# Optimization experiments

Hardware: AMD Instinct MI355X
Metric: run time of the kernel (lower is better)

## Reference

```python
import jax, jax.numpy as jnp
import numpy as np

# Binary (sign) weight linear: y = x @ sign(W)^T + b

def _binarize(w):
    # sign with sign(0) mapped to +1, as in typical BinaryLinear impls
    return jnp.where(w >= 0, 1.0, -1.0).astype(w.dtype)

def setup_inputs() -> dict:
    key = jax.random.key(0)
    ks = jax.random.split(key, 7)
    B = 65536
    x = jax.random.normal(ks[0], (B, 28, 28), dtype=jnp.float32)
    W1 = jax.random.normal(ks[1], (1000, 784), dtype=jnp.float32) * 0.05
    b1 = jax.random.normal(ks[2], (1000,), dtype=jnp.float32) * 0.01
    W2 = jax.random.normal(ks[3], (500, 1000), dtype=jnp.float32) * 0.05
    b2 = jax.random.normal(ks[4], (500,), dtype=jnp.float32) * 0.01
    W3 = jax.random.normal(ks[5], (10, 500), dtype=jnp.float32) * 0.05
    b3 = jax.random.normal(ks[6], (10,), dtype=jnp.float32) * 0.01
    return {"x": x, "W1": W1, "b1": b1, "W2": W2, "b2": b2, "W3": W3, "b3": b3}

def reference(x, W1, b1, W2, b2, W3, b3):
    h = x.reshape(x.shape[0], -1)                      # [B, 784]
    h = jnp.maximum(h @ _binarize(W1).T + b1, 0.0)     # [B, 1000]
    h = jnp.maximum(h @ _binarize(W2).T + b2, 0.0)     # [B, 500]
    return h @ _binarize(W3).T + b3                    # [B, 10]
```

## Files before the change

### kernel.cpp

```cpp
#include <hip/hip_runtime.h>
#include <stdint.h>


typedef __attribute__((ext_vector_type(8))) short bf16x8;
typedef __attribute__((ext_vector_type(4))) float f32x4;

typedef const __attribute__((address_space(1))) unsigned int* as1_u32p;
typedef __attribute__((address_space(3))) unsigned int* as3_u32p;

__device__ __forceinline__ void glds16(const void* g, void* l) {
  __builtin_amdgcn_global_load_lds((as1_u32p)g, (as3_u32p)l, 16, 0, 0);
}

__device__ __forceinline__ unsigned short f2bf(float f) {
  union { float f; unsigned u; } c;
  c.f = f;
  unsigned u = c.u;
  u += 0x7FFFu + ((u >> 16) & 1u);
  return (unsigned short)(u >> 16);
}

__device__ __forceinline__ void binarize_one(const float* __restrict__ src,
                                             int Ns, int Ks, short* __restrict__ dst,
                                             int Kp, int idx, int total) {
  if (idx >= total) return;
  int n = idx / Kp;
  int k = idx - n * Kp;
  short v = 0;
  if (n < Ns && k < Ks)
    v = (src[n * Ks + k] >= 0.0f) ? (short)0x3F80 : (short)0xBF80;
  dst[idx] = v;
}

__global__ void prep_kernel(const float* __restrict__ X, short* __restrict__ Xp,
                            const float* __restrict__ W1, short* __restrict__ W1b,
                            const float* __restrict__ W2, short* __restrict__ W2b,
                            const float* __restrict__ W3, short* __restrict__ W3b) {
  constexpr int C0 = 26624;
  constexpr int C1 = C0 + 3328;
  constexpr int C2 = C1 + 2048;
  const int bid = blockIdx.x;
  if (bid < C0) {
    const int g = bid * 256 + threadIdx.x;
    const int row = g / 104;
    const int c = (g - row * 104) * 8;
    short tmp[8];
    if (c < 784) {
      const float* s = X + (size_t)row * 784 + c;
      float4 f0 = *(const float4*)s;
      float4 f1 = *(const float4*)(s + 4);
      tmp[0] = (short)f2bf(f0.x); tmp[1] = (short)f2bf(f0.y);
      tmp[2] = (short)f2bf(f0.z); tmp[3] = (short)f2bf(f0.w);
      tmp[4] = (short)f2bf(f1.x); tmp[5] = (short)f2bf(f1.y);
      tmp[6] = (short)f2bf(f1.z); tmp[7] = (short)f2bf(f1.w);
    } else {
#pragma unroll
      for (int i = 0; i < 8; ++i) tmp[i] = 0;
    }
    *(bf16x8*)(Xp + (size_t)row * 832 + c) = *(bf16x8*)(tmp);
  } else if (bid < C1) {
    binarize_one(W1, 1000, 784, W1b, 832, (bid - C0) * 256 + threadIdx.x, 1024 * 832);
  } else if (bid < C2) {
    binarize_one(W2, 500, 1000, W2b, 1024, (bid - C1) * 256 + threadIdx.x, 512 * 1024);
  } else {
    binarize_one(W3, 10, 500, W3b, 512, (bid - C2) * 256 + threadIdx.x, 16 * 512);
  }
}

template <int KP, int NKT, int NP, int NR, int NT>
__global__ __launch_bounds__(512, 4)
void gemm128x256(const short* __restrict__ A, const short* __restrict__ Wb,
                 const float* __restrict__ bias, short* __restrict__ Hout) {
  __shared__ short Abuf[3][128 * 32];
  __shared__ short Bbuf[3][256 * 32];

  constexpr int NWG8 = (512 * NT) >> 3;
  const int d = blockIdx.x;
  const int lid = (d & 7) * NWG8 + (d >> 3);
  const int mi = lid / NT;
  const int ni = lid - mi * NT;
  const int m0 = mi << 7;
  const int n0 = ni << 8;
  const int start = (ni * NKT) / NT;

  const int tid = threadIdx.x;
  const int lane = tid & 63;
  const int w = tid >> 6;
  const int wm = w >> 2;
  const int wn = w & 3;
  const int l15 = lane & 15;
  const int quad = lane >> 4;

  const int srow = tid >> 2;
  const int sslot = tid & 3;
  const int gcol = ((sslot ^ ((srow >> 1) & 3)) << 3);
  const short* ag = A + (size_t)(m0 + srow) * KP + gcol;
  const short* bg = Wb + (size_t)(n0 + srow) * KP + gcol;
  const int ldsw = w << 9;

  auto stageA = [&](int pb, int kit) {
    glds16(ag + kit * 32, &Abuf[pb][ldsw]);
  };
  auto stageB = [&](int pb, int kit) {
    const short* s = bg + kit * 32;
    glds16(s, &Bbuf[pb][ldsw]);
    glds16(s + (size_t)128 * KP, &Bbuf[pb][ldsw + 4096]);
  };

  const int sl = (quad ^ ((l15 >> 1) & 3)) << 3;
  const int abase = ((wm << 6) + l15) * 32 + sl;
  const int bbase = ((wn << 6) + l15) * 32 + sl;

  f32x4 acc[4][4];
#pragma unroll
  for (int i = 0; i < 4; ++i)
#pragma unroll
    for (int j = 0; j < 4; ++j) acc[i][j] = (f32x4){0.f, 0.f, 0.f, 0.f};

  int kt1 = start + 1; if (kt1 >= NKT) kt1 -= NKT;
  stageA(0, start); stageB(0, start);
  stageA(1, kt1);   stageB(1, kt1);
  asm volatile("s_waitcnt vmcnt(3)" ::: "memory");
  __builtin_amdgcn_s_barrier();

  int pb = 0;
  int tb = 2;
  int kit2 = start + 2; if (kit2 >= NKT) kit2 -= NKT;

  for (int it = 0; it < NKT; ++it) {
    if (it + 2 < NKT) { stageA(tb, kit2); stageB(tb, kit2); }

    const short* Ab = &Abuf[pb][0];
    const short* Bb = &Bbuf[pb][0];
    bf16x8 af[4], bf[4];
#pragma unroll
    for (int i = 0; i < 4; ++i) af[i] = *(const bf16x8*)(Ab + abase + i * 512);
#pragma unroll
    for (int j = 0; j < 4; ++j) bf[j] = *(const bf16x8*)(Bb + bbase + j * 512);

    __builtin_amdgcn_s_setprio(1);
#pragma unroll
    for (int i = 0; i < 4; ++i)
#pragma unroll
      for (int j = 0; j < 4; ++j)
        acc[i][j] = __builtin_amdgcn_mfma_f32_16x16x32_bf16(af[i], bf[j], acc[i][j], 0, 0, 0);
    __builtin_amdgcn_s_setprio(0);

    if (it < NKT - 2) asm volatile("s_waitcnt vmcnt(3)" ::: "memory");
    else              asm volatile("s_waitcnt vmcnt(0)" ::: "memory");
    asm volatile("s_waitcnt lgkmcnt(0)" ::: "memory");
    __builtin_amdgcn_s_barrier();

    pb = (pb == 2) ? 0 : pb + 1;
    tb = (tb == 2) ? 0 : tb + 1;
    kit2 = kit2 + 1; if (kit2 >= NKT) kit2 -= NKT;
  }

  float bv[4];
#pragma unroll
  for (int j = 0; j < 4; ++j) {
    const int n = n0 + (wn << 6) + (j << 4) + l15;
    bv[j] = (n < NR) ? bias[n] : 0.f;
  }
#pragma unroll
  for (int i = 0; i < 4; ++i) {
#pragma unroll
    for (int r = 0; r < 4; ++r) {
      const int mr = m0 + (wm << 6) + (i << 4) + (quad << 2) + r;
      short* rowp = Hout + (size_t)mr * NP + n0 + (wn << 6) + l15;
#pragma unroll
      for (int j = 0; j < 4; ++j) {
        float v = acc[i][j][r] + bv[j];
        v = v > 0.f ? v : 0.f;
        rowp[j << 4] = (short)f2bf(v);
      }
    }
  }
}

__global__ __launch_bounds__(256, 2)
void gemm1_fused_kernel(const float* __restrict__ X, const short* __restrict__ Wb,
                        const float* __restrict__ bias, short* __restrict__ H) {
  constexpr int K = 784, KP = 832, NP = 1024, NR = 1000;
  __shared__ short As[128 * 32];
  __shared__ short Bs[128 * 32];

  const int tid = threadIdx.x;
  const int lane = tid & 63;
  const int wave = tid >> 6;
  const int wm = wave >> 1, wn = wave & 1;
  const int l15 = lane & 15;
  const int quad = lane >> 4;
  const int m0 = blockIdx.y * 128;
  const int n0 = blockIdx.x * 128;

  const int ar = tid >> 1;
  const int aks = (tid & 1) * 16;
  const float* xrow = X + (size_t)(m0 + ar) * K;
  short* adst = As + ar * 32 + aks;

  const int br = wave * 16 + (lane >> 2);
  const int bks = (lane & 3) * 8;
  const short* brow0 = Wb + (size_t)(n0 + br) * KP + bks;
  short* bdst = Bs + (wave * 16) * 32;

  f32x4 acc[4][4];
#pragma unroll
  for (int i = 0; i < 4; ++i)
#pragma unroll
    for (int j2 = 0; j2 < 4; ++j2) acc[i][j2] = (f32x4){0.f, 0.f, 0.f, 0.f};

  for (int k0 = 0; k0 < KP; k0 += 32) {
    glds16(brow0 + k0, bdst);
    glds16(brow0 + k0 + (size_t)64 * KP, bdst + 64 * 32);
    short tmp[16];
#pragma unroll
    for (int c = 0; c < 4; ++c) {
      const int kk = k0 + aks + c * 4;
      float4 f;
      if (kk + 3 < K)
        f = *(const float4*)(xrow + kk);
      else
        f = make_float4(0.f, 0.f, 0.f, 0.f);
      tmp[c * 4 + 0] = (short)f2bf(f.x);
      tmp[c * 4 + 1] = (short)f2bf(f.y);
      tmp[c * 4 + 2] = (short)f2bf(f.z);
      tmp[c * 4 + 3] = (short)f2bf(f.w);
    }
    *(bf16x8*)(adst) = *(bf16x8*)(tmp);
    *(bf16x8*)(adst + 8) = *(bf16x8*)(tmp + 8);
    __syncthreads();

    const short* abase = As + (size_t)(wm * 64 + l15) * 32 + quad * 8;
    const short* bbase = Bs + (size_t)(wn * 64 + l15) * 32 + quad * 8;
    bf16x8 af[4], bfr[4];
#pragma unroll
    for (int i = 0; i < 4; ++i) af[i] = *(const bf16x8*)(abase + i * 16 * 32);
#pragma unroll
    for (int j2 = 0; j2 < 4; ++j2) bfr[j2] = *(const bf16x8*)(bbase + j2 * 16 * 32);
#pragma unroll
    for (int i = 0; i < 4; ++i)
#pragma unroll
      for (int j2 = 0; j2 < 4; ++j2)
        acc[i][j2] = __builtin_amdgcn_mfma_f32_16x16x32_bf16(af[i], bfr[j2], acc[i][j2], 0, 0, 0);
    __syncthreads();
  }

#pragma unroll
  for (int j2 = 0; j2 < 4; ++j2) {
    const int n = n0 + wn * 64 + j2 * 16 + l15;
    const float bv = (n < NR) ? bias[n] : 0.f;
#pragma unroll
    for (int i = 0; i < 4; ++i) {
      const int mr = m0 + wm * 64 + i * 16 + quad * 4;
#pragma unroll
      for (int r = 0; r < 4; ++r) {
        float v = acc[i][j2][r] + bv;
        v = v > 0.f ? v : 0.f;
        H[(size_t)(mr + r) * NP + n] = (short)f2bf(v);
      }
    }
  }
}

__global__ __launch_bounds__(256, 2)
void gemm3_kernel(const short* __restrict__ Hin, const short* __restrict__ Wb,
                  const float* __restrict__ bias, float* __restrict__ Out) {
  constexpr int KP = 512;
  __shared__ short As[64 * KP];

  const int tid = threadIdx.x;
  const int lane = tid & 63;
  const int wave = tid >> 6;
  const int l15 = lane & 15;
  const int quad = lane >> 4;
  const int m0 = blockIdx.x * 64;

  bf16x8 bw[16];
#pragma unroll
  for (int kk = 0; kk < 16; ++kk)
    bw[kk] = *(const bf16x8*)(Wb + l15 * KP + kk * 32 + quad * 8);

  const short* asrc = Hin + (size_t)(m0 + wave * 16) * KP + lane * 8;
  short* adst = As + (size_t)(wave * 16) * KP;
#pragma unroll
  for (int t = 0; t < 16; ++t)
    glds16(asrc + (size_t)t * KP, adst + (size_t)t * KP);

  __syncthreads();

  f32x4 acc = (f32x4){0.f, 0.f, 0.f, 0.f};
  const short* abase = As + (size_t)(wave * 16 + l15) * KP + quad * 8;
#pragma unroll
  for (int kk = 0; kk < 16; ++kk) {
    bf16x8 af = *(const bf16x8*)(abase + kk * 32);
    acc = __builtin_amdgcn_mfma_f32_16x16x32_bf16(af, bw[kk], acc, 0, 0, 0);
  }

  if (l15 < 10) {
    const float bv = bias[l15];
#pragma unroll
    for (int r = 0; r < 4; ++r) {
      const int mr = m0 + wave * 16 + quad * 4 + r;
      Out[(size_t)mr * 10 + l15] = acc[r] + bv;
    }
  }
}

extern "C" void kernel_launch(void* const* d_in, const int* in_sizes, int n_in,
                              void* d_out, int out_size, void* d_ws, size_t ws_size,
                              hipStream_t stream) {
  const float* x = (const float*)d_in[0];
  const float* W1 = (const float*)d_in[1];
  const float* b1 = (const float*)d_in[2];
  const float* W2 = (const float*)d_in[3];
  const float* b2 = (const float*)d_in[4];
  const float* W3 = (const float*)d_in[5];
  const float* b3 = (const float*)d_in[6];
  float* out = (float*)d_out;

  const size_t szW1 = (size_t)1024 * 832 * 2;
  const size_t szW2 = (size_t)512 * 1024 * 2;
  const size_t szW3 = (size_t)16 * 512 * 2;
  const size_t szH1 = (size_t)65536 * 1024 * 2;
  const size_t szXp = (size_t)65536 * 832 * 2;
  const size_t need = szW1 + szW2 + szW3 + szH1 + szXp;

  uint8_t* p = (uint8_t*)d_ws;
  short* W1b = (short*)p; p += szW1;
  short* W2b = (short*)p; p += szW2;
  short* W3b = (short*)p; p += szW3;
  short* h1 = (short*)p; p += szH1;
  short* Z = (short*)p;

  if (ws_size >= need) {
    short* Xp = Z;
    short* h2 = Z;
    prep_kernel<<<26624 + 3328 + 2048 + 32, 256, 0, stream>>>(
        x, Xp, W1, W1b, W2, W2b, W3, W3b);
    gemm128x256<832, 26, 1024, 1000, 4><<<2048, 512, 0, stream>>>(Xp, W1b, b1, h1);
    gemm128x256<1024, 32, 512, 500, 2><<<1024, 512, 0, stream>>>(h1, W2b, b2, h2);
    gemm3_kernel<<<1024, 256, 0, stream>>>(h2, W3b, b3, out);
  } else {
    short* h2 = Z;
    prep_kernel<<<26624 + 3328 + 2048 + 32, 256, 0, stream>>>(
        x, Z ,
        W1, W1b, W2, W2b, W3, W3b);
    gemm1_fused_kernel<<<dim3(8, 512), 256, 0, stream>>>(x, W1b, b1, h1);
    gemm128x256<1024, 32, 512, 500, 2><<<1024, 512, 0, stream>>>(h1, W2b, b2, h2);
    gemm3_kernel<<<1024, 256, 0, stream>>>(h2, W3b, b3, out);
  }
}
```

Before: 529.4 us.

## Shrink GEMM tiles to 128x128 with 4 waves and double-buffered split-MFMA pipeline

Replaces the 128x256 tile GEMM using 8 waves and a triple-buffered LDS ring with a 128x128 tile using 4 waves and double buffering. The next stage's global-to-LDS loads are issued mid-iteration, between the two halves of the MFMA block, after a barrier. Smaller tiles double the grid size and cut LDS per block, which may raise occupancy. The cost is lower arithmetic intensity per tile (more global traffic for W and activations) and an extra barrier per K step.

```diff
diff --git a/kernel.cpp b/kernel.cpp
--- a/kernel.cpp
+++ b/kernel.cpp
@@ -68,11 +68,11 @@
 }
 
 template <int KP, int NKT, int NP, int NR, int NT>
-__global__ __launch_bounds__(512, 4)
-void gemm128x256(const short* __restrict__ A, const short* __restrict__ Wb,
-                 const float* __restrict__ bias, short* __restrict__ Hout) {
-  __shared__ short Abuf[3][128 * 32];
-  __shared__ short Bbuf[3][256 * 32];
+__global__ __launch_bounds__(256, 4)
+void gemm128(const short* __restrict__ A, const short* __restrict__ Wb,
+             const float* __restrict__ bias, short* __restrict__ Hout) {
+  __shared__ short Abuf[2][128 * 32];
+  __shared__ short Bbuf[2][128 * 32];
 
   constexpr int NWG8 = (512 * NT) >> 3;
   const int d = blockIdx.x;
@@ -80,31 +80,30 @@
   const int mi = lid / NT;
   const int ni = lid - mi * NT;
   const int m0 = mi << 7;
-  const int n0 = ni << 8;
+  const int n0 = ni << 7;
   const int start = (ni * NKT) / NT;
 
   const int tid = threadIdx.x;
   const int lane = tid & 63;
   const int w = tid >> 6;
-  const int wm = w >> 2;
-  const int wn = w & 3;
+  const int wm = w >> 1;
+  const int wn = w & 1;
   const int l15 = lane & 15;
   const int quad = lane >> 4;
 
   const int srow = tid >> 2;
-  const int sslot = tid & 3;
-  const int gcol = ((sslot ^ ((srow >> 1) & 3)) << 3);
+  const int gcol = (((tid & 3) ^ ((srow >> 1) & 3)) << 3);
   const short* ag = A + (size_t)(m0 + srow) * KP + gcol;
   const short* bg = Wb + (size_t)(n0 + srow) * KP + gcol;
   const int ldsw = w << 9;
 
-  auto stageA = [&](int pb, int kit) {
-    glds16(ag + kit * 32, &Abuf[pb][ldsw]);
-  };
-  auto stageB = [&](int pb, int kit) {
-    const short* s = bg + kit * 32;
-    glds16(s, &Bbuf[pb][ldsw]);
-    glds16(s + (size_t)128 * KP, &Bbuf[pb][ldsw + 4096]);
+  auto stage = [&](int pb, int kit) {
+    const short* sa = ag + kit * 32;
+    const short* sb = bg + kit * 32;
+    glds16(sa, &Abuf[pb][ldsw]);
+    glds16(sa + (size_t)64 * KP, &Abuf[pb][ldsw + 2048]);
+    glds16(sb, &Bbuf[pb][ldsw]);
+    glds16(sb + (size_t)64 * KP, &Bbuf[pb][ldsw + 2048]);
   };
 
   const int sl = (quad ^ ((l15 >> 1) & 3)) << 3;
@@ -118,20 +117,18 @@
     for (int j = 0; j < 4; ++j) acc[i][j] = (f32x4){0.f, 0.f, 0.f, 0.f};
 
   int kt1 = start + 1; if (kt1 >= NKT) kt1 -= NKT;
-  stageA(0, start); stageB(0, start);
-  stageA(1, kt1);   stageB(1, kt1);
-  asm volatile("s_waitcnt vmcnt(3)" ::: "memory");
+  stage(0, start);
+  stage(1, kt1);
+  asm volatile("s_waitcnt vmcnt(4)" ::: "memory");
   __builtin_amdgcn_s_barrier();
 
-  int pb = 0;
-  int tb = 2;
-  int kit2 = start + 2; if (kit2 >= NKT) kit2 -= NKT;
-
   for (int it = 0; it < NKT; ++it) {
-    if (it + 2 < NKT) { stageA(tb, kit2); stageB(tb, kit2); }
-
+    const int pb = it & 1;
     const short* Ab = &Abuf[pb][0];
     const short* Bb = &Bbuf[pb][0];
+    int kit2 = start + it + 2; if (kit2 >= NKT) kit2 -= NKT;
+    const bool stg = (it + 2 < NKT);
+
     bf16x8 af[4], bf[4];
 #pragma unroll
     for (int i = 0; i < 4; ++i) af[i] = *(const bf16x8*)(Ab + abase + i * 512);
@@ -140,20 +137,25 @@
 
     __builtin_amdgcn_s_setprio(1);
 #pragma unroll
-    for (int i = 0; i < 4; ++i)
+    for (int i = 0; i < 2; ++i)
 #pragma unroll
       for (int j = 0; j < 4; ++j)
         acc[i][j] = __builtin_amdgcn_mfma_f32_16x16x32_bf16(af[i], bf[j], acc[i][j], 0, 0, 0);
     __builtin_amdgcn_s_setprio(0);
-
-    if (it < NKT - 2) asm volatile("s_waitcnt vmcnt(3)" ::: "memory");
-    else              asm volatile("s_waitcnt vmcnt(0)" ::: "memory");
     asm volatile("s_waitcnt lgkmcnt(0)" ::: "memory");
     __builtin_amdgcn_s_barrier();
 
-    pb = (pb == 2) ? 0 : pb + 1;
-    tb = (tb == 2) ? 0 : tb + 1;
-    kit2 = kit2 + 1; if (kit2 >= NKT) kit2 -= NKT;
+    if (stg) stage(pb, kit2);
+    __builtin_amdgcn_s_setprio(1);
+#pragma unroll
+    for (int i = 2; i < 4; ++i)
+#pragma unroll
+      for (int j = 0; j < 4; ++j)
+        acc[i][j] = __builtin_amdgcn_mfma_f32_16x16x32_bf16(af[i], bf[j], acc[i][j], 0, 0, 0);
+    __builtin_amdgcn_s_setprio(0);
+    if (stg) asm volatile("s_waitcnt vmcnt(4)" ::: "memory");
+    else     asm volatile("s_waitcnt vmcnt(0)" ::: "memory");
+    __builtin_amdgcn_s_barrier();
   }
 
   float bv[4];
@@ -338,16 +340,15 @@
     short* h2 = Z;
     prep_kernel<<<26624 + 3328 + 2048 + 32, 256, 0, stream>>>(
         x, Xp, W1, W1b, W2, W2b, W3, W3b);
-    gemm128x256<832, 26, 1024, 1000, 4><<<2048, 512, 0, stream>>>(Xp, W1b, b1, h1);
-    gemm128x256<1024, 32, 512, 500, 2><<<1024, 512, 0, stream>>>(h1, W2b, b2, h2);
+    gemm128<832, 26, 1024, 1000, 8><<<4096, 256, 0, stream>>>(Xp, W1b, b1, h1);
+    gemm128<1024, 32, 512, 500, 4><<<2048, 256, 0, stream>>>(h1, W2b, b2, h2);
     gemm3_kernel<<<1024, 256, 0, stream>>>(h2, W3b, b3, out);
   } else {
     short* h2 = Z;
     prep_kernel<<<26624 + 3328 + 2048 + 32, 256, 0, stream>>>(
-        x, Z ,
-        W1, W1b, W2, W2b, W3, W3b);
+        x, Z, W1, W1b, W2, W2b, W3, W3b);
     gemm1_fused_kernel<<<dim3(8, 512), 256, 0, stream>>>(x, W1b, b1, h1);
-    gemm128x256<1024, 32, 512, 500, 2><<<1024, 512, 0, stream>>>(h1, W2b, b2, h2);
+    gemm128<1024, 32, 512, 500, 4><<<2048, 256, 0, stream>>>(h1, W2b, b2, h2);
     gemm3_kernel<<<1024, 256, 0, stream>>>(h2, W3b, b3, out);
   }
 }
```

New measurement: 560.3 us. 5.8% more time.
